# Performance work log

Hardware: AMD Instinct MI355X
Metric: run time of the kernel (lower is better)

## Reference

```python
import jax, jax.numpy as jnp
import numpy as np

N = 50000      # nodes
E = 800000     # edges (avg degree 16)
IN = 256       # in_dim == heads*hidden (so DGL residual is Identity)
H = 4          # heads
D = 64         # hidden_dim / out_dim per head
EPS = 1e-5
NEG_SLOPE_ATTN = 0.2   # DGL GATConv edge-attention leaky_relu slope
NEG_SLOPE_ACT = 0.01   # F.leaky_relu default


def gat_conv(x, src, dst, W, al, ar, b, act):
    # x: [N, H*D], W: [H*D, H*D], al/ar: [H, D], b: [H*D]
    feat = (x @ W).reshape(N, H, D)                       # [N,H,D]
    el = jnp.sum(feat * al, axis=-1)                      # [N,H]
    er = jnp.sum(feat * ar, axis=-1)                      # [N,H]
    e = jax.nn.leaky_relu(el[src] + er[dst], NEG_SLOPE_ATTN)  # [E,H]
    # segment softmax over incoming edges per destination node
    m = jax.ops.segment_max(e, dst, num_segments=N)       # [N,H]
    m = jnp.where(jnp.isfinite(m), m, 0.0)                # nodes with no in-edges
    ee = jnp.exp(e - m[dst])                              # [E,H]
    denom = jax.ops.segment_sum(ee, dst, num_segments=N)  # [N,H]
    alpha = ee / jnp.maximum(denom[dst], 1e-9)            # [E,H]
    msg = feat[src] * alpha[:, :, None]                   # [E,H,D]
    rst = jax.ops.segment_sum(msg, dst, num_segments=N)   # [N,H,D]
    rst = rst + x.reshape(N, H, D)                        # identity residual (dims match)
    rst = rst + b.reshape(1, H, D)
    if act:
        rst = jax.nn.leaky_relu(rst, NEG_SLOPE_ACT)
    return rst


def batch_norm(h, gamma, beta):
    # BatchNorm1d in training mode: batch statistics over node dim
    mu = jnp.mean(h, axis=0)
    var = jnp.var(h, axis=0)
    return (h - mu) * jax.lax.rsqrt(var + EPS) * gamma + beta


def setup_inputs():
    key = jax.random.key(0)
    ks = jax.random.split(key, 18)
    s = 1.0 / np.sqrt(IN)
    inp = {
        'x': jax.random.normal(ks[0], (N, IN), jnp.float32),
        'src': jax.random.randint(ks[1], (E,), 0, N),
        'dst': jax.random.randint(ks[2], (E,), 0, N),
    }
    names = ['W1', 'al1', 'ar1', 'b1', 'W2', 'al2', 'ar2', 'b2', 'W3', 'al3', 'ar3', 'b3']
    shapes = [(IN, H * D), (H, D), (H, D), (H * D,)] * 3
    for i, (nm, sh) in enumerate(zip(names, shapes)):
        inp[nm] = jax.random.normal(ks[3 + i], sh, jnp.float32) * s
    inp['g1'] = jnp.ones((H * D,), jnp.float32)
    inp['be1'] = jnp.zeros((H * D,), jnp.float32)
    inp['g2'] = jnp.ones((H * D,), jnp.float32)
    inp['be2'] = jnp.zeros((H * D,), jnp.float32)
    return inp


def reference(x, src, dst, W1, al1, ar1, b1, W2, al2, ar2, b2, W3, al3, ar3, b3, g1, be1, g2, be2):
    h = gat_conv(x, src, dst, W1, al1, ar1, b1, act=True).reshape(N, H * D)
    h = batch_norm(h, g1, be1)
    h = gat_conv(h, src, dst, W2, al2, ar2, b2, act=True).reshape(N, H * D)
    h = batch_norm(h, g2, be2)
    h = gat_conv(h, src, dst, W3, al3, ar3, b3, act=False)   # [N,H,D]
    return h.mean(axis=1)                                    # [N,D]
```

## Files before the change

### kernel.cpp

```cpp
#include <hip/hip_runtime.h>

constexpr int NN = 50000;
constexpr int NE = 800000;
constexpr float SLOPE_A = 0.2f;
constexpr float SLOPE_R = 0.01f;
constexpr int SCB = 196;

typedef __attribute__((ext_vector_type(8))) short bf16x8;
typedef __attribute__((ext_vector_type(4))) float f32x4;

__device__ __forceinline__ unsigned short f2bf(float f) {
    union { float f; unsigned u; } v; v.f = f;
    unsigned u = v.u;
    unsigned r = u + 0x7fffu + ((u >> 16) & 1u);
    return (unsigned short)(r >> 16);
}
__device__ __forceinline__ float bf2f(unsigned short s) {
    union { unsigned u; float f; } v; v.u = ((unsigned)s) << 16;
    return v.f;
}

__global__ void k_hist(const int* __restrict__ dst, int* __restrict__ cnt) {
    int i = blockIdx.x * 256 + threadIdx.x;
    if (i < NE) atomicAdd(&cnt[dst[i]], 1);
}

__global__ void k_scan1(const int* __restrict__ cnt, int* __restrict__ loc,
                        int* __restrict__ bsum) {
    __shared__ int sh[256];
    int t = threadIdx.x;
    int i = blockIdx.x * 256 + t;
    int v = (i < NN) ? cnt[i] : 0;
    sh[t] = v;
    __syncthreads();
    for (int off = 1; off < 256; off <<= 1) {
        int tmp = (t >= off) ? sh[t - off] : 0;
        __syncthreads();
        sh[t] += tmp;
        __syncthreads();
    }
    loc[i] = sh[t] - v;
    if (t == 255) bsum[blockIdx.x] = sh[255];
}

__global__ void k_scan2(const int* __restrict__ bsum, int* __restrict__ boff,
                        int* __restrict__ rowptr) {
    __shared__ int sh[256];
    int t = threadIdx.x;
    int v = (t < SCB) ? bsum[t] : 0;
    sh[t] = v;
    __syncthreads();
    for (int off = 1; off < 256; off <<= 1) {
        int tmp = (t >= off) ? sh[t - off] : 0;
        __syncthreads();
        sh[t] += tmp;
        __syncthreads();
    }
    if (t < SCB) boff[t] = sh[t] - v;
    if (t == 255) rowptr[NN] = sh[255];
}

__global__ void k_scan3(const int* __restrict__ loc, const int* __restrict__ boff,
                        int* __restrict__ rowptr, int* __restrict__ cursor) {
    int i = blockIdx.x * 256 + threadIdx.x;
    if (i < NN) {
        int r = loc[i] + boff[blockIdx.x];
        rowptr[i] = r;
        cursor[i] = r;
    }
}

__global__ void k_scatter(const int* __restrict__ src, const int* __restrict__ dst,
                          int* __restrict__ cursor, int* __restrict__ ssrc) {
    int i = blockIdx.x * 256 + threadIdx.x;
    if (i < NE) {
        int d = dst[i];
        int pos = atomicAdd(&cursor[d], 1);
        ssrc[pos] = src[i];
    }
}

__global__ void k_prepw(const float* __restrict__ W1, const float* __restrict__ W2,
                        const float* __restrict__ W3, unsigned short* __restrict__ Wt) {
    int b = blockIdx.x;
    int L = b >> 8, k = b & 255;
    const float* W = (L == 0) ? W1 : ((L == 1) ? W2 : W3);
    int j = threadIdx.x;
    Wt[L * 65536 + j * 256 + k] = f2bf(W[k * 256 + j]);
}

__global__ void k_xcast(const float* __restrict__ x, unsigned short* __restrict__ xbf) {
    size_t i = (size_t)blockIdx.x * 256 + threadIdx.x;
    float4 v = *(const float4*)(x + i * 4);
    ushort4 p;
    p.x = f2bf(v.x); p.y = f2bf(v.y); p.z = f2bf(v.z); p.w = f2bf(v.w);
    *(ushort4*)(xbf + i * 4) = p;
}

__global__ void k_fold(const unsigned short* __restrict__ Wsrc, const float* __restrict__ sc,
                       const float* __restrict__ sh, unsigned short* __restrict__ Wt2,
                       float* __restrict__ cvec) {
    __shared__ float red[256];
    int j = blockIdx.x, k = threadIdx.x;
    float w = bf2f(Wsrc[j * 256 + k]);
    float s = sc ? sc[k] : 1.f;
    float hs = sh ? sh[k] : 0.f;
    Wt2[j * 256 + k] = f2bf(s * w);
    red[k] = hs * w;
    __syncthreads();
    for (int off = 128; off > 0; off >>= 1) {
        if (k < off) red[k] += red[k + off];
        __syncthreads();
    }
    if (k == 0) cvec[j] = red[0];
}

__launch_bounds__(256, 2)
__global__ void k_gemm(const unsigned short* __restrict__ A, const unsigned short* __restrict__ Wt,
                       const float* __restrict__ cvec,
                       const float* __restrict__ al, const float* __restrict__ ar,
                       unsigned short* __restrict__ feat16, float* __restrict__ el,
                       float* __restrict__ er) {
    constexpr int AP = 264;
    __shared__ __align__(16) unsigned short Alds[64 * AP];
    const int tid = threadIdx.x;
    const int rowbase = blockIdx.x * 64;

    for (int it = 0; it < 8; it++) {
        int idx = it * 256 + tid;
        int rr = idx >> 5;
        int c16 = idx & 31;
        int gr = rowbase + rr;
        uint4 v = make_uint4(0u, 0u, 0u, 0u);
        if (gr < NN) v = *(const uint4*)(A + (size_t)gr * 256 + c16 * 8);
        *(uint4*)(&Alds[rr * AP + c16 * 8]) = v;
    }
    __syncthreads();

    f32x4 acc[4][4];
    for (int i = 0; i < 4; i++)
        for (int j = 0; j < 4; j++)
            acc[i][j] = (f32x4){0.f, 0.f, 0.f, 0.f};

    const int lane = tid & 63, w = tid >> 6;
    const int mm = lane & 15, q = lane >> 4;

    const unsigned short* bbase = Wt + ((size_t)(64 * w + mm)) * 256 + q * 8;

#pragma unroll
    for (int kc = 0; kc < 8; kc++) {
        bf16x8 a[4], b[4];
        for (int i = 0; i < 4; i++)
            a[i] = *(const bf16x8*)(&Alds[(16 * i + mm) * AP + kc * 32 + q * 8]);
        for (int j = 0; j < 4; j++)
            b[j] = *(const bf16x8*)(bbase + j * (16 * 256) + kc * 32);
        for (int i = 0; i < 4; i++)
            for (int j = 0; j < 4; j++)
                acc[i][j] = __builtin_amdgcn_mfma_f32_16x16x32_bf16(a[i], b[j], acc[i][j], 0, 0, 0);
    }

    float cv[4];
    for (int j = 0; j < 4; j++) cv[j] = cvec[64 * w + 16 * j + mm];
    for (int i = 0; i < 4; i++)
        for (int j = 0; j < 4; j++)
            for (int r = 0; r < 4; r++)
                acc[i][j][r] += cv[j];

    float alv[4], arv[4];
    for (int j = 0; j < 4; j++) {
        alv[j] = al[w * 64 + 16 * j + mm];
        arv[j] = ar[w * 64 + 16 * j + mm];
    }
    for (int i = 0; i < 4; i++) {
        for (int r = 0; r < 4; r++) {
            int gr = rowbase + 16 * i + q * 4 + r;
            float se = 0.f, sr = 0.f;
            for (int j = 0; j < 4; j++) {
                se += acc[i][j][r] * alv[j];
                sr += acc[i][j][r] * arv[j];
            }
            for (int off = 1; off < 16; off <<= 1) {
                se += __shfl_xor(se, off, 64);
                sr += __shfl_xor(sr, off, 64);
            }
            if (mm == 0 && gr < NN) {
                el[gr * 4 + w] = se;
                er[gr * 4 + w] = sr;
            }
        }
    }

    for (int i = 0; i < 4; i++) {
        for (int j = 0; j < 4; j++) {
            int gc = 64 * w + 16 * j + mm;
            for (int r = 0; r < 4; r++) {
                int gr = rowbase + 16 * i + q * 4 + r;
                if (gr < NN) feat16[(size_t)gr * 256 + gc] = f2bf(acc[i][j][r]);
            }
        }
    }
}

__launch_bounds__(256)
__global__ void k_agg(const unsigned short* __restrict__ feat16, const float* __restrict__ el,
                      const float* __restrict__ er, const int* __restrict__ rowptr,
                      const int* __restrict__ ssrc, const unsigned short* __restrict__ resid,
                      const float* __restrict__ bnscale, const float* __restrict__ bnshift,
                      int use_bn, const float* __restrict__ bias, int act,
                      unsigned short* __restrict__ outh, float* __restrict__ outf,
                      int final_mean) {
    int n = __builtin_amdgcn_readfirstlane(blockIdx.x * 4 + (threadIdx.x >> 6));
    int l = threadIdx.x & 63;
    int h = l >> 4;
    int beg = rowptr[n], end = rowptr[n + 1];
    float erh = er[n * 4 + h];

    float d = 0.f;
    float4 acc = make_float4(0.f, 0.f, 0.f, 0.f);

    for (int e = beg; e < end; e += 8) {
        int ss[8];
        float cc[8];
        ushort4 ff[8];
#pragma unroll
        for (int j = 0; j < 8; j++) {
            int ee = e + j;
            ss[j] = ssrc[(ee < end) ? ee : beg];
        }
#pragma unroll
        for (int j = 0; j < 8; j++)
            cc[j] = el[ss[j] * 4 + h];
#pragma unroll
        for (int j = 0; j < 8; j++)
            ff[j] = *(const ushort4*)(feat16 + (size_t)ss[j] * 256 + l * 4);
#pragma unroll
        for (int j = 0; j < 8; j++) {
            float sc = cc[j] + erh;
            sc = (sc > 0.f) ? sc : SLOPE_A * sc;
            float wgt = ((e + j) < end) ? __expf(sc) : 0.f;
            d += wgt;
            acc.x += bf2f(ff[j].x) * wgt;
            acc.y += bf2f(ff[j].y) * wgt;
            acc.z += bf2f(ff[j].z) * wgt;
            acc.w += bf2f(ff[j].w) * wgt;
        }
    }

    float invd = 1.f / fmaxf(d, 1e-9f);
    acc.x *= invd; acc.y *= invd; acc.z *= invd; acc.w *= invd;

    ushort4 rv = *(const ushort4*)(resid + (size_t)n * 256 + l * 4);
    float4 r = make_float4(bf2f(rv.x), bf2f(rv.y), bf2f(rv.z), bf2f(rv.w));
    if (use_bn) {
        float4 sc4 = *(const float4*)(bnscale + l * 4);
        float4 sh4 = *(const float4*)(bnshift + l * 4);
        r.x = r.x * sc4.x + sh4.x;
        r.y = r.y * sc4.y + sh4.y;
        r.z = r.z * sc4.z + sh4.z;
        r.w = r.w * sc4.w + sh4.w;
    }
    float4 bb = *(const float4*)(bias + l * 4);
    acc.x += r.x + bb.x; acc.y += r.y + bb.y;
    acc.z += r.z + bb.z; acc.w += r.w + bb.w;
    if (act) {
        acc.x = (acc.x > 0.f) ? acc.x : SLOPE_R * acc.x;
        acc.y = (acc.y > 0.f) ? acc.y : SLOPE_R * acc.y;
        acc.z = (acc.z > 0.f) ? acc.z : SLOPE_R * acc.z;
        acc.w = (acc.w > 0.f) ? acc.w : SLOPE_R * acc.w;
    }

    if (!final_mean) {
        ushort4 p;
        p.x = f2bf(acc.x); p.y = f2bf(acc.y); p.z = f2bf(acc.z); p.w = f2bf(acc.w);
        *(ushort4*)(outh + (size_t)n * 256 + l * 4) = p;
    } else {
        acc.x += __shfl_xor(acc.x, 16, 64); acc.x += __shfl_xor(acc.x, 32, 64);
        acc.y += __shfl_xor(acc.y, 16, 64); acc.y += __shfl_xor(acc.y, 32, 64);
        acc.z += __shfl_xor(acc.z, 16, 64); acc.z += __shfl_xor(acc.z, 32, 64);
        acc.w += __shfl_xor(acc.w, 16, 64); acc.w += __shfl_xor(acc.w, 32, 64);
        if (l < 16) {
            acc.x *= 0.25f; acc.y *= 0.25f; acc.z *= 0.25f; acc.w *= 0.25f;
            *(float4*)(outf + (size_t)n * 64 + l * 4) = acc;
        }
    }
}

__global__ void k_bnstats(const unsigned short* __restrict__ hh, float* __restrict__ sums) {
    int t = threadIdx.x;
    int b = blockIdx.x;
    int r0 = b * 196, r1 = min(r0 + 196, NN);
    float s = 0.f, s2 = 0.f;
    for (int r = r0; r < r1; r++) {
        float v = bf2f(hh[(size_t)r * 256 + t]);
        s += v; s2 += v * v;
    }
    atomicAdd(&sums[t], s);
    atomicAdd(&sums[256 + t], s2);
}

__global__ void k_bnfinal(const float* __restrict__ sums, const float* __restrict__ g,
                          const float* __restrict__ be, float* __restrict__ scale,
                          float* __restrict__ shift) {
    int t = threadIdx.x;
    float mu = sums[t] * (1.f / NN);
    float var = sums[256 + t] * (1.f / NN) - mu * mu;
    float rs = rsqrtf(var + 1e-5f);
    float sc = rs * g[t];
    scale[t] = sc;
    shift[t] = be[t] - mu * sc;
}

extern "C" void kernel_launch(void* const* d_in, const int* in_sizes, int n_in,
                              void* d_out, int out_size, void* d_ws, size_t ws_size,
                              hipStream_t stream) {
    const float* x   = (const float*)d_in[0];
    const int* src   = (const int*)d_in[1];
    const int* dst   = (const int*)d_in[2];
    const float* W1  = (const float*)d_in[3];
    const float* al1 = (const float*)d_in[4];
    const float* ar1 = (const float*)d_in[5];
    const float* b1  = (const float*)d_in[6];
    const float* W2  = (const float*)d_in[7];
    const float* al2 = (const float*)d_in[8];
    const float* ar2 = (const float*)d_in[9];
    const float* b2  = (const float*)d_in[10];
    const float* W3  = (const float*)d_in[11];
    const float* al3 = (const float*)d_in[12];
    const float* ar3 = (const float*)d_in[13];
    const float* b3  = (const float*)d_in[14];
    const float* g1  = (const float*)d_in[15];
    const float* be1 = (const float*)d_in[16];
    const float* g2  = (const float*)d_in[17];
    const float* be2 = (const float*)d_in[18];
    float* out = (float*)d_out;

    char* ws = (char*)d_ws;
    size_t off = 0;
    auto alloc = [&](size_t bytes) {
        void* p = ws + off;
        off += (bytes + 255) & ~(size_t)255;
        return p;
    };
    int* rowptr = (int*)alloc((NN + 1) * sizeof(int));
    int* cursor = (int*)alloc(NN * sizeof(int));
    int* cnt    = (int*)alloc(SCB * 256 * sizeof(int));
    int* loc    = (int*)alloc(SCB * 256 * sizeof(int));
    int* bsum   = (int*)alloc(SCB * sizeof(int));
    int* boff   = (int*)alloc(SCB * sizeof(int));
    int* ssrc   = (int*)alloc(NE * sizeof(int));
    unsigned short* xbf    = (unsigned short*)alloc((size_t)NN * 256 * sizeof(unsigned short));
    unsigned short* feat16 = (unsigned short*)alloc((size_t)NN * 256 * sizeof(unsigned short));
    unsigned short* hbuf   = (unsigned short*)alloc((size_t)NN * 256 * sizeof(unsigned short));
    float* el   = (float*)alloc((size_t)NN * 4 * sizeof(float));
    float* er   = (float*)alloc((size_t)NN * 4 * sizeof(float));
    unsigned short* Wt  = (unsigned short*)alloc(3 * 65536 * sizeof(unsigned short));
    unsigned short* Wt2 = (unsigned short*)alloc(65536 * sizeof(unsigned short));
    float* cvec    = (float*)alloc(256 * sizeof(float));
    float* bnsums  = (float*)alloc(512 * sizeof(float));
    float* bnscale = (float*)alloc(256 * sizeof(float));
    float* bnshift = (float*)alloc(256 * sizeof(float));

    hipMemsetAsync(cnt, 0, NN * sizeof(int), stream);
    k_xcast<<<12500, 256, 0, stream>>>(x, xbf);
    k_hist<<<(NE + 255) / 256, 256, 0, stream>>>(dst, cnt);
    k_scan1<<<SCB, 256, 0, stream>>>(cnt, loc, bsum);
    k_scan2<<<1, 256, 0, stream>>>(bsum, boff, rowptr);
    k_scan3<<<SCB, 256, 0, stream>>>(loc, boff, rowptr, cursor);
    k_scatter<<<(NE + 255) / 256, 256, 0, stream>>>(src, dst, cursor, ssrc);
    k_prepw<<<768, 256, 0, stream>>>(W1, W2, W3, Wt);

    const int GB = (NN + 63) / 64;
    const int NB = NN / 4;

    k_fold<<<256, 256, 0, stream>>>(Wt, nullptr, nullptr, Wt2, cvec);
    k_gemm<<<GB, 256, 0, stream>>>(xbf, Wt2, cvec, al1, ar1, feat16, el, er);
    k_agg<<<NB, 256, 0, stream>>>(feat16, el, er, rowptr, ssrc, xbf,
                                  nullptr, nullptr, 0, b1, 1, hbuf, nullptr, 0);
    hipMemsetAsync(bnsums, 0, 512 * sizeof(float), stream);
    k_bnstats<<<256, 256, 0, stream>>>(hbuf, bnsums);
    k_bnfinal<<<1, 256, 0, stream>>>(bnsums, g1, be1, bnscale, bnshift);

    k_fold<<<256, 256, 0, stream>>>(Wt + 65536, bnscale, bnshift, Wt2, cvec);
    k_gemm<<<GB, 256, 0, stream>>>(hbuf, Wt2, cvec, al2, ar2, feat16, el, er);
    k_agg<<<NB, 256, 0, stream>>>(feat16, el, er, rowptr, ssrc, hbuf,
                                  bnscale, bnshift, 1, b2, 1, hbuf, nullptr, 0);
    hipMemsetAsync(bnsums, 0, 512 * sizeof(float), stream);
    k_bnstats<<<256, 256, 0, stream>>>(hbuf, bnsums);
    k_bnfinal<<<1, 256, 0, stream>>>(bnsums, g2, be2, bnscale, bnshift);

    k_fold<<<256, 256, 0, stream>>>(Wt + 131072, bnscale, bnshift, Wt2, cvec);
    k_gemm<<<GB, 256, 0, stream>>>(hbuf, Wt2, cvec, al3, ar3, feat16, el, er);
    k_agg<<<NB, 256, 0, stream>>>(feat16, el, er, rowptr, ssrc, hbuf,
                                  bnscale, bnshift, 1, b3, 0, nullptr, out, 1);
}
```

Before: 629.8 us.

## Fuse input cast into GEMM, pre-swizzle weight fragments, split edge loop across two waves

Removes the separate fp32-to-bf16 cast kernel by having the first GEMM load fp32 x directly and convert on the fly, and the first aggregation reads the fp32 residual. Weights are rearranged into MFMA fragment order so each lane's B loads are contiguous. GEMM output is staged through LDS for coalesced 16-byte stores. Aggregation uses two waves per node, each taking alternate groups of 8 edges and combining partial sums in shared memory, which raises parallelism but adds a block barrier.

Result: faster. 610.1 us (-3.1%).

```diff
diff --git a/kernel.cpp b/kernel.cpp
--- a/kernel.cpp
+++ b/kernel.cpp
@@ -89,34 +89,46 @@
     Wt[L * 65536 + j * 256 + k] = f2bf(W[k * 256 + j]);
 }
 
-__global__ void k_xcast(const float* __restrict__ x, unsigned short* __restrict__ xbf) {
-    size_t i = (size_t)blockIdx.x * 256 + threadIdx.x;
-    float4 v = *(const float4*)(x + i * 4);
-    ushort4 p;
-    p.x = f2bf(v.x); p.y = f2bf(v.y); p.z = f2bf(v.z); p.w = f2bf(v.w);
-    *(ushort4*)(xbf + i * 4) = p;
-}
-
-__global__ void k_fold(const unsigned short* __restrict__ Wsrc, const float* __restrict__ sc,
-                       const float* __restrict__ sh, unsigned short* __restrict__ Wt2,
+__global__ void k_fold(const unsigned short* __restrict__ Wt, const float* __restrict__ sc,
+                       const float* __restrict__ sh, unsigned short* __restrict__ Wfrag,
                        float* __restrict__ cvec) {
-    __shared__ float red[256];
-    int j = blockIdx.x, k = threadIdx.x;
-    float w = bf2f(Wsrc[j * 256 + k]);
-    float s = sc ? sc[k] : 1.f;
-    float hs = sh ? sh[k] : 0.f;
-    Wt2[j * 256 + k] = f2bf(s * w);
-    red[k] = hs * w;
-    __syncthreads();
-    for (int off = 128; off > 0; off >>= 1) {
-        if (k < off) red[k] += red[k + off];
+    int b = blockIdx.x;
+    if (b < 512) {
+        int gid = b * 256 + threadIdx.x;
+        int lane = gid & 63;
+        int frag = gid >> 6;
+        int j = frag & 3, kc = (frag >> 2) & 7, w = frag >> 5;
+        int mm = lane & 15, q = lane >> 4;
+        int n = 64 * w + 16 * j + mm;
+        int k0 = kc * 32 + q * 8;
+        const unsigned short* srcp = Wt + n * 256 + k0;
+        unsigned short o[8];
+        if (sc) {
+#pragma unroll
+            for (int t = 0; t < 8; t++)
+                o[t] = f2bf(sc[k0 + t] * bf2f(srcp[t]));
+        } else {
+#pragma unroll
+            for (int t = 0; t < 8; t++) o[t] = srcp[t];
+        }
+        *(uint4*)(Wfrag + (size_t)gid * 8) = *(const uint4*)o;
+    } else {
+        __shared__ float red[256];
+        int n = b - 512;
+        int k = threadIdx.x;
+        red[k] = sh[k] * bf2f(Wt[n * 256 + k]);
         __syncthreads();
-    }
-    if (k == 0) cvec[j] = red[0];
+        for (int off = 128; off > 0; off >>= 1) {
+            if (k < off) red[k] += red[k + off];
+            __syncthreads();
+        }
+        if (k == 0) cvec[n] = red[0];
+    }
 }
 
 __launch_bounds__(256, 2)
-__global__ void k_gemm(const unsigned short* __restrict__ A, const unsigned short* __restrict__ Wt,
+__global__ void k_gemm(const void* __restrict__ Araw, int af32,
+                       const unsigned short* __restrict__ Wfrag,
                        const float* __restrict__ cvec,
                        const float* __restrict__ al, const float* __restrict__ ar,
                        unsigned short* __restrict__ feat16, float* __restrict__ el,
@@ -126,14 +138,30 @@
     const int tid = threadIdx.x;
     const int rowbase = blockIdx.x * 64;
 
-    for (int it = 0; it < 8; it++) {
-        int idx = it * 256 + tid;
-        int rr = idx >> 5;
-        int c16 = idx & 31;
-        int gr = rowbase + rr;
-        uint4 v = make_uint4(0u, 0u, 0u, 0u);
-        if (gr < NN) v = *(const uint4*)(A + (size_t)gr * 256 + c16 * 8);
-        *(uint4*)(&Alds[rr * AP + c16 * 8]) = v;
+    if (af32) {
+        const float* A = (const float*)Araw;
+        int r = tid >> 6;
+        int c4 = tid & 63;
+        for (int it = 0; it < 16; it++) {
+            int rr = it * 4 + r;
+            int gr = rowbase + rr;
+            float4 v = make_float4(0.f, 0.f, 0.f, 0.f);
+            if (gr < NN) v = *(const float4*)(A + (size_t)gr * 256 + c4 * 4);
+            ushort4 pv;
+            pv.x = f2bf(v.x); pv.y = f2bf(v.y); pv.z = f2bf(v.z); pv.w = f2bf(v.w);
+            *(ushort4*)(&Alds[rr * AP + c4 * 4]) = pv;
+        }
+    } else {
+        const unsigned short* A = (const unsigned short*)Araw;
+        for (int it = 0; it < 8; it++) {
+            int idx = it * 256 + tid;
+            int rr = idx >> 5;
+            int c16 = idx & 31;
+            int gr = rowbase + rr;
+            uint4 v = make_uint4(0u, 0u, 0u, 0u);
+            if (gr < NN) v = *(const uint4*)(A + (size_t)gr * 256 + c16 * 8);
+            *(uint4*)(&Alds[rr * AP + c16 * 8]) = v;
+        }
     }
     __syncthreads();
 
@@ -145,7 +173,7 @@
     const int lane = tid & 63, w = tid >> 6;
     const int mm = lane & 15, q = lane >> 4;
 
-    const unsigned short* bbase = Wt + ((size_t)(64 * w + mm)) * 256 + q * 8;
+    const unsigned short* bbase = Wfrag + ((size_t)w * 8 * 4) * 512 + (size_t)lane * 8;
 
 #pragma unroll
     for (int kc = 0; kc < 8; kc++) {
@@ -153,18 +181,21 @@
         for (int i = 0; i < 4; i++)
             a[i] = *(const bf16x8*)(&Alds[(16 * i + mm) * AP + kc * 32 + q * 8]);
         for (int j = 0; j < 4; j++)
-            b[j] = *(const bf16x8*)(bbase + j * (16 * 256) + kc * 32);
+            b[j] = *(const bf16x8*)(bbase + (size_t)(kc * 4 + j) * 512);
         for (int i = 0; i < 4; i++)
             for (int j = 0; j < 4; j++)
                 acc[i][j] = __builtin_amdgcn_mfma_f32_16x16x32_bf16(a[i], b[j], acc[i][j], 0, 0, 0);
     }
-
-    float cv[4];
-    for (int j = 0; j < 4; j++) cv[j] = cvec[64 * w + 16 * j + mm];
-    for (int i = 0; i < 4; i++)
-        for (int j = 0; j < 4; j++)
-            for (int r = 0; r < 4; r++)
-                acc[i][j][r] += cv[j];
+    __syncthreads();
+
+    if (cvec) {
+        float cv[4];
+        for (int j = 0; j < 4; j++) cv[j] = cvec[64 * w + 16 * j + mm];
+        for (int i = 0; i < 4; i++)
+            for (int j = 0; j < 4; j++)
+                for (int r = 0; r < 4; r++)
+                    acc[i][j][r] += cv[j];
+    }
 
     float alv[4], arv[4];
     for (int j = 0; j < 4; j++) {
@@ -190,27 +221,40 @@
         }
     }
 
-    for (int i = 0; i < 4; i++) {
+    for (int i = 0; i < 4; i++)
         for (int j = 0; j < 4; j++) {
             int gc = 64 * w + 16 * j + mm;
             for (int r = 0; r < 4; r++) {
-                int gr = rowbase + 16 * i + q * 4 + r;
-                if (gr < NN) feat16[(size_t)gr * 256 + gc] = f2bf(acc[i][j][r]);
+                int rr = 16 * i + q * 4 + r;
+                Alds[rr * AP + gc] = f2bf(acc[i][j][r]);
             }
         }
+    __syncthreads();
+    for (int it = 0; it < 8; it++) {
+        int idx = it * 256 + tid;
+        int rr = idx >> 5;
+        int c16 = idx & 31;
+        int gr = rowbase + rr;
+        if (gr < NN)
+            *(uint4*)(feat16 + (size_t)gr * 256 + c16 * 8) = *(const uint4*)(&Alds[rr * AP + c16 * 8]);
     }
 }
 
 __launch_bounds__(256)
 __global__ void k_agg(const unsigned short* __restrict__ feat16, const float* __restrict__ el,
                       const float* __restrict__ er, const int* __restrict__ rowptr,
-                      const int* __restrict__ ssrc, const unsigned short* __restrict__ resid,
+                      const int* __restrict__ ssrc,
+                      const unsigned short* __restrict__ residh, const float* __restrict__ residf,
                       const float* __restrict__ bnscale, const float* __restrict__ bnshift,
                       int use_bn, const float* __restrict__ bias, int act,
                       unsigned short* __restrict__ outh, float* __restrict__ outf,
                       int final_mean) {
-    int n = __builtin_amdgcn_readfirstlane(blockIdx.x * 4 + (threadIdx.x >> 6));
-    int l = threadIdx.x & 63;
+    __shared__ float comb[2][64][5];
+    int tid = threadIdx.x;
+    int nl = tid >> 7;
+    int v = (tid >> 6) & 1;
+    int l = tid & 63;
+    int n = __builtin_amdgcn_readfirstlane(blockIdx.x * 2 + nl);
     int h = l >> 4;
     int beg = rowptr[n], end = rowptr[n + 1];
     float erh = er[n * 4 + h];
@@ -218,7 +262,7 @@
     float d = 0.f;
     float4 acc = make_float4(0.f, 0.f, 0.f, 0.f);
 
-    for (int e = beg; e < end; e += 8) {
+    for (int e = beg + 8 * v; e < end; e += 16) {
         int ss[8];
         float cc[8];
         ushort4 ff[8];
@@ -246,11 +290,27 @@
         }
     }
 
+    if (v == 1) {
+        comb[nl][l][0] = acc.x; comb[nl][l][1] = acc.y;
+        comb[nl][l][2] = acc.z; comb[nl][l][3] = acc.w;
+        comb[nl][l][4] = d;
+    }
+    __syncthreads();
+    if (v == 1) return;
+    acc.x += comb[nl][l][0]; acc.y += comb[nl][l][1];
+    acc.z += comb[nl][l][2]; acc.w += comb[nl][l][3];
+    d += comb[nl][l][4];
+
     float invd = 1.f / fmaxf(d, 1e-9f);
     acc.x *= invd; acc.y *= invd; acc.z *= invd; acc.w *= invd;
 
-    ushort4 rv = *(const ushort4*)(resid + (size_t)n * 256 + l * 4);
-    float4 r = make_float4(bf2f(rv.x), bf2f(rv.y), bf2f(rv.z), bf2f(rv.w));
+    float4 r;
+    if (residf) {
+        r = *(const float4*)(residf + (size_t)n * 256 + l * 4);
+    } else {
+        ushort4 rv = *(const ushort4*)(residh + (size_t)n * 256 + l * 4);
+        r = make_float4(bf2f(rv.x), bf2f(rv.y), bf2f(rv.z), bf2f(rv.w));
+    }
     if (use_bn) {
         float4 sc4 = *(const float4*)(bnscale + l * 4);
         float4 sh4 = *(const float4*)(bnshift + l * 4);
@@ -348,48 +408,47 @@
     int* bsum   = (int*)alloc(SCB * sizeof(int));
     int* boff   = (int*)alloc(SCB * sizeof(int));
     int* ssrc   = (int*)alloc(NE * sizeof(int));
-    unsigned short* xbf    = (unsigned short*)alloc((size_t)NN * 256 * sizeof(unsigned short));
     unsigned short* feat16 = (unsigned short*)alloc((size_t)NN * 256 * sizeof(unsigned short));
     unsigned short* hbuf   = (unsigned short*)alloc((size_t)NN * 256 * sizeof(unsigned short));
     float* el   = (float*)alloc((size_t)NN * 4 * sizeof(float));
     float* er   = (float*)alloc((size_t)NN * 4 * sizeof(float));
-    unsigned short* Wt  = (unsigned short*)alloc(3 * 65536 * sizeof(unsigned short));
-    unsigned short* Wt2 = (unsigned short*)alloc(65536 * sizeof(unsigned short));
+    unsigned short* Wt     = (unsigned short*)alloc(3 * 65536 * sizeof(unsigned short));
+    unsigned short* Wfrag1 = (unsigned short*)alloc(131072 * sizeof(unsigned short) * 8);
+    unsigned short* Wfrag2 = (unsigned short*)alloc(131072 * sizeof(unsigned short) * 8);
     float* cvec    = (float*)alloc(256 * sizeof(float));
     float* bnsums  = (float*)alloc(512 * sizeof(float));
     float* bnscale = (float*)alloc(256 * sizeof(float));
     float* bnshift = (float*)alloc(256 * sizeof(float));
 
     hipMemsetAsync(cnt, 0, NN * sizeof(int), stream);
-    k_xcast<<<12500, 256, 0, stream>>>(x, xbf);
     k_hist<<<(NE + 255) / 256, 256, 0, stream>>>(dst, cnt);
     k_scan1<<<SCB, 256, 0, stream>>>(cnt, loc, bsum);
     k_scan2<<<1, 256, 0, stream>>>(bsum, boff, rowptr);
     k_scan3<<<SCB, 256, 0, stream>>>(loc, boff, rowptr, cursor);
     k_scatter<<<(NE + 255) / 256, 256, 0, stream>>>(src, dst, cursor, ssrc);
     k_prepw<<<768, 256, 0, stream>>>(W1, W2, W3, Wt);
+    k_fold<<<512, 256, 0, stream>>>(Wt, nullptr, nullptr, Wfrag1, nullptr);
 
     const int GB = (NN + 63) / 64;
-    const int NB = NN / 4;
-
-    k_fold<<<256, 256, 0, stream>>>(Wt, nullptr, nullptr, Wt2, cvec);
-    k_gemm<<<GB, 256, 0, stream>>>(xbf, Wt2, cvec, al1, ar1, feat16, el, er);
-    k_agg<<<NB, 256, 0, stream>>>(feat16, el, er, rowptr, ssrc, xbf,
+    const int NB = NN / 2;
+
+    k_gemm<<<GB, 256, 0, stream>>>(x, 1, Wfrag1, nullptr, al1, ar1, feat16, el, er);
+    k_agg<<<NB, 256, 0, stream>>>(feat16, el, er, rowptr, ssrc, nullptr, x,
                                   nullptr, nullptr, 0, b1, 1, hbuf, nullptr, 0);
     hipMemsetAsync(bnsums, 0, 512 * sizeof(float), stream);
     k_bnstats<<<256, 256, 0, stream>>>(hbuf, bnsums);
     k_bnfinal<<<1, 256, 0, stream>>>(bnsums, g1, be1, bnscale, bnshift);
-
-    k_fold<<<256, 256, 0, stream>>>(Wt + 65536, bnscale, bnshift, Wt2, cvec);
-    k_gemm<<<GB, 256, 0, stream>>>(hbuf, Wt2, cvec, al2, ar2, feat16, el, er);
-    k_agg<<<NB, 256, 0, stream>>>(feat16, el, er, rowptr, ssrc, hbuf,
+    k_fold<<<768, 256, 0, stream>>>(Wt + 65536, bnscale, bnshift, Wfrag2, cvec);
+
+    k_gemm<<<GB, 256, 0, stream>>>(hbuf, 0, Wfrag2, cvec, al2, ar2, feat16, el, er);
+    k_agg<<<NB, 256, 0, stream>>>(feat16, el, er, rowptr, ssrc, hbuf, nullptr,
                                   bnscale, bnshift, 1, b2, 1, hbuf, nullptr, 0);
     hipMemsetAsync(bnsums, 0, 512 * sizeof(float), stream);
     k_bnstats<<<256, 256, 0, stream>>>(hbuf, bnsums);
     k_bnfinal<<<1, 256, 0, stream>>>(bnsums, g2, be2, bnscale, bnshift);
-
-    k_fold<<<256, 256, 0, stream>>>(Wt + 131072, bnscale, bnshift, Wt2, cvec);
-    k_gemm<<<GB, 256, 0, stream>>>(hbuf, Wt2, cvec, al3, ar3, feat16, el, er);
-    k_agg<<<NB, 256, 0, stream>>>(feat16, el, er, rowptr, ssrc, hbuf,
+    k_fold<<<768, 256, 0, stream>>>(Wt + 131072, bnscale, bnshift, Wfrag2, cvec);
+
+    k_gemm<<<GB, 256, 0, stream>>>(hbuf, 0, Wfrag2, cvec, al3, ar3, feat16, el, er);
+    k_agg<<<NB, 256, 0, stream>>>(feat16, el, er, rowptr, ssrc, hbuf, nullptr,
                                   bnscale, bnshift, 1, b3, 0, nullptr, out, 1);
 }
```
